# Kernel optimization log

Measured on AMD Instinct MI355X. Metric: run time of the kernel, lower is better.

The kernel has to match this reference:

```python
import jax, jax.numpy as jnp
import numpy as np

B, L, N, D, C, WS, NH = 32, 64, 1024, 512, 8192, 3, 16
HD = D // NH          # head_dim = 32
HID = 2 * D           # MLP expansion = 2


def _ln(x, g, b, eps=1e-5):
    m = jnp.mean(x, -1, keepdims=True)
    v = jnp.mean((x - m) ** 2, -1, keepdims=True)
    return (x - m) * jax.lax.rsqrt(v + eps) * g + b


def setup_inputs() -> dict:
    key = jax.random.key(0)
    ks = jax.random.split(key, 16)
    r = lambda i, shape, s=0.02: jax.random.normal(ks[i], shape, jnp.float32) * s
    return dict(
        visual_features=jax.random.normal(ks[0], (B, N, D), jnp.float32),
        targets=jax.random.randint(ks[1], (B, L), 0, C),
        pad_id=1,
        char_embed=r(2, (C, D), 1.0),
        ln1_g=jnp.ones(D), ln1_b=jnp.zeros(D),
        in_proj_w=r(3, (3 * D, D)), in_proj_b=jnp.zeros(3 * D),
        out_w=r(4, (D, D)), out_b=jnp.zeros(D),
        fc1_w=r(5, (HID, D)), fc1_b=jnp.zeros(HID),
        fc2_w=r(6, (D, HID)), fc2_b=jnp.zeros(D),
        ln2_g=jnp.ones(D), ln2_b=jnp.zeros(D),
        left_token=r(7, (1, 1, D)), right_token=r(8, (1, 1, D)),
        q_w=r(9, (D, D)), q_b=jnp.zeros(D),
        kv_w=r(10, (2 * D, D)), kv_b=jnp.zeros(2 * D),
        proj_w=r(11, (D, D)), proj_b=jnp.zeros(D),
        lnq_g=jnp.ones(D), lnq_b=jnp.zeros(D),
        lnkv_g=jnp.ones(D), lnkv_b=jnp.zeros(D),
        head_w=r(12, (C, D)), head_b=jnp.zeros(C),
    )


def reference(visual_features, targets, pad_id, char_embed, ln1_g, ln1_b,
              in_proj_w, in_proj_b, out_w, out_b, fc1_w, fc1_b, fc2_w, fc2_b,
              ln2_g, ln2_b, left_token, right_token, q_w, q_b, kv_w, kv_b,
              proj_w, proj_b, lnq_g, lnq_b, lnkv_g, lnkv_b, head_w, head_b):
    # --- build left/right context windows via gather (vectorizes the python loop) ---
    padded = jnp.pad(targets, ((0, 0), (WS, WS)), constant_values=pad_id)
    li = jnp.arange(L)[:, None] + jnp.arange(WS)[None, :]      # (L, WS)
    left_ids = padded[:, li]                                   # (B, L, WS)
    right_ids = padded[:, li + WS + 1]                         # (B, L, WS)

    def encode(ids, tok):
        x = char_embed[ids] + tok                 # (B, L, WS, D)
        x = x.reshape(B * L, WS, D)               # (M, WS, D)
        xn = _ln(x, ln1_g, ln1_b)
        qkv = xn @ in_proj_w.T + in_proj_b
        q, k, v = jnp.split(qkv, 3, -1)
        sh = lambda t: t.reshape(B * L, WS, NH, HD).transpose(0, 2, 1, 3)
        q, k, v = sh(q), sh(k), sh(v)
        a = jax.nn.softmax(jnp.einsum('mhqd,mhkd->mhqk', q, k) * HD ** -0.5, -1)
        o = jnp.einsum('mhqk,mhkd->mhqd', a, v).transpose(0, 2, 1, 3).reshape(B * L, WS, D)
        x = x + o @ out_w.T + out_b
        h = jax.nn.gelu(_ln(x, ln2_g, ln2_b) @ fc1_w.T + fc1_b, approximate=False)
        x = x + h @ fc2_w.T + fc2_b
        return x.mean(1).reshape(B, L, D)

    def cross(qs):
        q = _ln(qs, lnq_g, lnq_b) @ q_w.T + q_b
        kv = _ln(visual_features, lnkv_g, lnkv_b) @ kv_w.T + kv_b
        k, v = jnp.split(kv, 2, -1)
        q = q.reshape(B, L, NH, HD).transpose(0, 2, 1, 3)
        k = k.reshape(B, N, NH, HD).transpose(0, 2, 1, 3)
        v = v.reshape(B, N, NH, HD).transpose(0, 2, 1, 3)
        a = jax.nn.softmax(jnp.einsum('bhld,bhnd->bhln', q, k) * HD ** -0.5, -1)
        o = jnp.einsum('bhln,bhnd->bhld', a, v).transpose(0, 2, 1, 3).reshape(B, L, D)
        return o @ proj_w.T + proj_b

    left_enc = encode(left_ids, left_token)
    right_enc = encode(right_ids, right_token)
    left_feat = left_enc + cross(left_enc)
    right_feat = right_enc + cross(right_enc)
    sgm_left = left_feat @ head_w.T + head_b      # (B, L, C)
    sgm_right = right_feat @ head_w.T + head_b    # (B, L, C)
    return sgm_left, sgm_right, targets
```

## Files before the change

### kernel.cpp

```cpp
#include <hip/hip_runtime.h>
#include <hip/hip_bf16.h>
#include <cstdint>
#include <cstddef>


typedef __attribute__((ext_vector_type(8))) short s16x8;
typedef __attribute__((ext_vector_type(8))) unsigned short u16x8;
typedef __attribute__((ext_vector_type(4))) unsigned short u16x4;
typedef __attribute__((ext_vector_type(4))) float f32x4;

__device__ __forceinline__ float b2f(unsigned short u) {
  union { unsigned int i; float f; } c; c.i = ((unsigned int)u) << 16; return c.f;
}
__device__ __forceinline__ unsigned short f2b(float f) {
  union { float f; unsigned int i; } c; c.f = f;
  unsigned int x = c.i;
  return (unsigned short)((x + 0x7FFFu + ((x >> 16) & 1u)) >> 16);
}

#define GLOAD16(gp, lp)                                                        \
  __builtin_amdgcn_global_load_lds(                                           \
      (const __attribute__((address_space(1))) void*)(gp),                    \
      (__attribute__((address_space(3))) void*)(lp), 16, 0, 0)

__global__ void cvt_f32_bf16(const float* __restrict__ s, unsigned short* __restrict__ d, int n4) {
  int i = blockIdx.x * 256 + threadIdx.x;
  if (i >= n4) return;
  float4 v = ((const float4*)s)[i];
  u16x4 o; o[0] = f2b(v.x); o[1] = f2b(v.y); o[2] = f2b(v.z); o[3] = f2b(v.w);
  *(u16x4*)(d + (size_t)i * 4) = o;
}

__global__ void embed_k(const int* __restrict__ targets, const int* __restrict__ pad_p,
                        const float* __restrict__ ce, const float* __restrict__ ltok,
                        const float* __restrict__ rtok, unsigned short* __restrict__ x) {
  int idx = blockIdx.x * 256 + threadIdx.x;
  if (idx >= 12288 * 128) return;
  int row = idx >> 7, d4 = idx & 127;
  int side = row >= 6144;
  int rem = row - side * 6144;
  int pos = rem / 3, w = rem - pos * 3;
  int b = pos >> 6, l = pos & 63;
  int id;
  if (!side) { int ti = l + w - 3; id = (ti >= 0) ? targets[(b << 6) + ti] : *pad_p; }
  else       { int ti = l + w + 1; id = (ti < 64) ? targets[(b << 6) + ti] : *pad_p; }
  float4 cv = ((const float4*)ce)[(size_t)id * 128 + d4];
  float4 tv = ((const float4*)(side ? rtok : ltok))[d4];
  u16x4 o; o[0] = f2b(cv.x + tv.x); o[1] = f2b(cv.y + tv.y);
  o[2] = f2b(cv.z + tv.z); o[3] = f2b(cv.w + tv.w);
  *(u16x4*)(x + (size_t)idx * 4) = o;
}

template<int INBF>
__global__ __launch_bounds__(256) void ln_rows(const void* __restrict__ in,
    const float* __restrict__ g, const float* __restrict__ b,
    unsigned short* __restrict__ out, int M) {
  int row = blockIdx.x * 4 + (threadIdx.x >> 6);
  int lane = threadIdx.x & 63;
  float vv[8];
  if (INBF) {
    u16x8 v8 = *(const u16x8*)((const unsigned short*)in + (size_t)row * 512 + lane * 8);
#pragma unroll
    for (int j = 0; j < 8; ++j) vv[j] = b2f(v8[j]);
  } else {
    const float* rp = (const float*)in + (size_t)row * 512;
    float4 v0 = ((const float4*)rp)[lane * 2];
    float4 v1 = ((const float4*)rp)[lane * 2 + 1];
    vv[0] = v0.x; vv[1] = v0.y; vv[2] = v0.z; vv[3] = v0.w;
    vv[4] = v1.x; vv[5] = v1.y; vv[6] = v1.z; vv[7] = v1.w;
  }
  float s = 0.f, ss = 0.f;
#pragma unroll
  for (int j = 0; j < 8; ++j) { s += vv[j]; ss += vv[j] * vv[j]; }
#pragma unroll
  for (int o = 1; o < 64; o <<= 1) { s += __shfl_xor(s, o); ss += __shfl_xor(ss, o); }
  float mean = s * (1.0f / 512.0f);
  float var = ss * (1.0f / 512.0f) - mean * mean;
  float inv = rsqrtf(var + 1e-5f);
  int c = lane * 8;
  u16x8 o8;
#pragma unroll
  for (int j = 0; j < 8; ++j) o8[j] = f2b((vv[j] - mean) * inv * g[c + j] + b[c + j]);
  *(u16x8*)(out + (size_t)row * 512 + c) = o8;
}

template<int RES, int GELU, int OUTBF, int KVT>
__global__ __launch_bounds__(256) void gemm128(
    const unsigned short* __restrict__ A, const unsigned short* __restrict__ Bt,
    const float* __restrict__ bias, const void* __restrict__ res,
    void* __restrict__ outp, int M, int N, int K) {
  __shared__ unsigned short sA[2][8192];
  __shared__ unsigned short sB[2][8192];
  const int tid = threadIdx.x;
  const int nbx = gridDim.x, nby = gridDim.y;
  int id = blockIdx.y * nbx + blockIdx.x;
  {
    const int nwg = nbx * nby;
    if ((nwg & 7) == 0) id = (id & 7) * (nwg >> 3) + (id >> 3);
  }
  int bm, bn;
  if (nbx >= nby) { bm = (id % nby) * 128; bn = (id / nby) * 128; }
  else            { bm = (id / nbx) * 128; bn = (id % nbx) * 128; }
  const int wave = tid >> 6, lane = tid & 63;
  const int wr = (wave >> 1) * 64, wc = (wave & 1) * 64;
  const int lrow = lane & 15, g = lane >> 4;
  f32x4 acc[4][4] = {};
  const int xoff = (((((lrow & 1) << 2) | g) ^ ((lrow >> 1) & 7)) << 3);
  const int baseA = ((wr >> 1) + (lrow >> 1)) * 64 + xoff;
  const int baseB = ((wc >> 1) + (lrow >> 1)) * 64 + xoff;
  const int slot8 = (tid & 7) ^ ((tid >> 3) & 7);
  const int srow = ((tid >> 3) << 1) + (slot8 >> 2);
  const int scol = (slot8 & 3) << 3;
  const unsigned short* gA = A + (size_t)(bm + srow) * K + scol;
  const unsigned short* gB = Bt + (size_t)(bn + srow) * K + scol;
  const int NT = K >> 6;

#define STAGE128(buf, kt)                                                      \
  { _Pragma("unroll")                                                          \
    for (int h = 0; h < 2; ++h) {                                              \
      _Pragma("unroll")                                                        \
      for (int i = 0; i < 2; ++i) {                                            \
        GLOAD16(gA + (size_t)(i * 64) * K + (kt) * 64 + h * 32,                \
                &sA[buf][h * 4096 + i * 2048 + wave * 512]);                   \
        GLOAD16(gB + (size_t)(i * 64) * K + (kt) * 64 + h * 32,                \
                &sB[buf][h * 4096 + i * 2048 + wave * 512]);                   \
      }                                                                        \
    } }

  STAGE128(0, 0);
  __syncthreads();
  int cur = 0;
  for (int kt = 0; kt < NT; ++kt) {
    s16x8 a0[4], b0[4];
#pragma unroll
    for (int m = 0; m < 4; ++m) a0[m] = *(const s16x8*)&sA[cur][baseA + m * 512];
#pragma unroll
    for (int n = 0; n < 4; ++n) b0[n] = *(const s16x8*)&sB[cur][baseB + n * 512];
    if (kt + 1 < NT) STAGE128(cur ^ 1, kt + 1);
    __builtin_amdgcn_s_setprio(1);
#pragma unroll
    for (int m = 0; m < 4; ++m)
#pragma unroll
      for (int n = 0; n < 4; ++n)
        acc[m][n] = __builtin_amdgcn_mfma_f32_16x16x32_bf16(b0[n], a0[m], acc[m][n], 0, 0, 0);
    __builtin_amdgcn_s_setprio(0);
    s16x8 a1[4], b1[4];
#pragma unroll
    for (int m = 0; m < 4; ++m) a1[m] = *(const s16x8*)&sA[cur][4096 + baseA + m * 512];
#pragma unroll
    for (int n = 0; n < 4; ++n) b1[n] = *(const s16x8*)&sB[cur][4096 + baseB + n * 512];
    __builtin_amdgcn_s_setprio(1);
#pragma unroll
    for (int m = 0; m < 4; ++m)
#pragma unroll
      for (int n = 0; n < 4; ++n)
        acc[m][n] = __builtin_amdgcn_mfma_f32_16x16x32_bf16(b1[n], a1[m], acc[m][n], 0, 0, 0);
    __builtin_amdgcn_s_setprio(0);
    __syncthreads();
    cur ^= 1;
  }
#undef STAGE128

  const int orow_ = bm + wr + lrow;
  const int ocol_ = bn + wc + g * 4;
#pragma unroll
  for (int m = 0; m < 4; ++m) {
    const int row = orow_ + m * 16;
#pragma unroll
    for (int n = 0; n < 4; ++n) {
      const int col = ocol_ + n * 16;
      f32x4 v = acc[m][n];
      f32x4 b4 = *(const f32x4*)(bias + col);
      v += b4;
      if (GELU) {
#pragma unroll
        for (int r = 0; r < 4; ++r)
          v[r] = 0.5f * v[r] * (1.0f + erff(v[r] * 0.70710678118654752f));
      }
      if (RES == 1) v += *(const f32x4*)((const float*)res + (size_t)row * N + col);
      if (RES == 2) {
        u16x4 r4 = *(const u16x4*)((const unsigned short*)res + (size_t)row * N + col);
#pragma unroll
        for (int r = 0; r < 4; ++r) v[r] += b2f(r4[r]);
      }
      if (KVT) {
        int bb = row >> 10, nn = row & 1023;
        unsigned short* Kp = (unsigned short*)outp;
        unsigned short* VpT = Kp + 16777216u;
        if (col < 512) {
          int hh = col >> 5, dd = col & 31;
          u16x4 o4;
#pragma unroll
          for (int r = 0; r < 4; ++r) o4[r] = f2b(v[r]);
          *(u16x4*)(Kp + (((size_t)(bb * 16 + hh)) * 1024 + nn) * 32 + dd) = o4;
        } else {
          int cc = col - 512, hh = cc >> 5, dd = cc & 31;
#pragma unroll
          for (int r = 0; r < 4; ++r)
            VpT[(((size_t)(bb * 16 + hh)) * 32 + dd + r) * 1024 + nn] = f2b(v[r]);
        }
      } else if (OUTBF) {
        u16x4 o4;
#pragma unroll
        for (int r = 0; r < 4; ++r) o4[r] = f2b(v[r]);
        *(u16x4*)((unsigned short*)outp + (size_t)row * N + col) = o4;
      } else {
        *(f32x4*)((float*)outp + (size_t)row * N + col) = v;
      }
    }
  }
}

__global__ __launch_bounds__(256) void winattn(const unsigned short* __restrict__ qkv,
                                               unsigned short* __restrict__ o) {
  int g = blockIdx.x * 256 + threadIdx.x;
  if (g >= 4096 * 48) return;
  int i = g % 3;
  int t = g / 3;
  int h = t & 15;
  int sp = t >> 4;
  const unsigned short* base = qkv + (size_t)sp * 4608 + h * 32;
  float qv[32];
  {
    const u16x8* qp = (const u16x8*)(base + (size_t)i * 1536);
#pragma unroll
    for (int c = 0; c < 4; ++c) {
      u16x8 v = qp[c];
#pragma unroll
      for (int j = 0; j < 8; ++j) qv[c * 8 + j] = b2f(v[j]);
    }
  }
  float s[3];
#pragma unroll
  for (int j3 = 0; j3 < 3; ++j3) {
    const u16x8* kp = (const u16x8*)(base + (size_t)j3 * 1536 + 512);
    float acc = 0.f;
#pragma unroll
    for (int c = 0; c < 4; ++c) {
      u16x8 v = kp[c];
#pragma unroll
      for (int j = 0; j < 8; ++j) acc += qv[c * 8 + j] * b2f(v[j]);
    }
    s[j3] = acc * 0.17677669529663687f;
  }
  float mx = fmaxf(s[0], fmaxf(s[1], s[2]));
  float e0 = __expf(s[0] - mx), e1 = __expf(s[1] - mx), e2 = __expf(s[2] - mx);
  float inv = 1.0f / (e0 + e1 + e2);
  float a0 = e0 * inv, a1 = e1 * inv, a2 = e2 * inv;
  unsigned short* op = o + (size_t)(sp * 3 + i) * 512 + h * 32;
  const u16x8* v0p = (const u16x8*)(base + 1024);
  const u16x8* v1p = (const u16x8*)(base + 1536 + 1024);
  const u16x8* v2p = (const u16x8*)(base + 3072 + 1024);
#pragma unroll
  for (int c = 0; c < 4; ++c) {
    u16x8 x0 = v0p[c], x1 = v1p[c], x2 = v2p[c];
    u16x8 ov;
#pragma unroll
    for (int j = 0; j < 8; ++j)
      ov[j] = f2b(a0 * b2f(x0[j]) + a1 * b2f(x1[j]) + a2 * b2f(x2[j]));
    *(u16x8*)(op + c * 8) = ov;
  }
}

__global__ void mean3(const unsigned short* __restrict__ x, float* __restrict__ enc) {
  int i = blockIdx.x * 256 + threadIdx.x;
  if (i >= 4096 * 128) return;
  int p = i >> 7, d4 = i & 127;
  u16x4 a = *(const u16x4*)(x + ((size_t)(p * 3 + 0) * 512 + d4 * 4));
  u16x4 b = *(const u16x4*)(x + ((size_t)(p * 3 + 1) * 512 + d4 * 4));
  u16x4 c = *(const u16x4*)(x + ((size_t)(p * 3 + 2) * 512 + d4 * 4));
  float4 o;
  o.x = (b2f(a[0]) + b2f(b[0]) + b2f(c[0])) * (1.0f / 3.0f);
  o.y = (b2f(a[1]) + b2f(b[1]) + b2f(c[1])) * (1.0f / 3.0f);
  o.z = (b2f(a[2]) + b2f(b[2]) + b2f(c[2])) * (1.0f / 3.0f);
  o.w = (b2f(a[3]) + b2f(b[3]) + b2f(c[3])) * (1.0f / 3.0f);
  ((float4*)enc)[i] = o;
}

__global__ __launch_bounds__(256) void crossattn_mfma(const unsigned short* __restrict__ q,
    const unsigned short* __restrict__ Kp, const unsigned short* __restrict__ VpT,
    unsigned short* __restrict__ o) {
  __shared__ unsigned short Plds[4][2][16 * 40];
  const int sbh = blockIdx.x;
  const int side = sbh >> 9, b = (sbh >> 4) & 31, h = sbh & 15;
  const int tid = threadIdx.x;
  const int w = tid >> 6, lane = tid & 63;
  const int ql = lane & 15, g = lane >> 4;
  const int qrow = side * 2048 + b * 64 + w * 16 + ql;
  const float SC = 0.17677669529663687f;
  s16x8 qf;
  {
    u16x8 qv8 = *(const u16x8*)(q + (size_t)qrow * 512 + h * 32 + g * 8);
#pragma unroll
    for (int j = 0; j < 8; ++j) qf[j] = (short)f2b(b2f(qv8[j]) * SC);
  }
  const unsigned short* kbase = Kp + ((size_t)(b * 16 + h) * 1024) * 32;
  const unsigned short* vbase = VpT + ((size_t)(b * 16 + h) * 32) * 1024;
  f32x4 oacc0 = {}, oacc1 = {};
  float m_run = -1e30f, l_part = 0.f;
  for (int kv0 = 0; kv0 < 1024; kv0 += 32) {
    const int pp = (kv0 >> 5) & 1;
    s16x8 kf0 = *(const s16x8*)(kbase + (size_t)(kv0 + ql) * 32 + g * 8);
    s16x8 kf1 = *(const s16x8*)(kbase + (size_t)(kv0 + 16 + ql) * 32 + g * 8);
    f32x4 z = {0.f, 0.f, 0.f, 0.f};
    f32x4 s0 = __builtin_amdgcn_mfma_f32_16x16x32_bf16(kf0, qf, z, 0, 0, 0);
    f32x4 s1 = __builtin_amdgcn_mfma_f32_16x16x32_bf16(kf1, qf, z, 0, 0, 0);
    float cm = fmaxf(fmaxf(fmaxf(s0[0], s0[1]), fmaxf(s0[2], s0[3])),
                     fmaxf(fmaxf(s1[0], s1[1]), fmaxf(s1[2], s1[3])));
    cm = fmaxf(cm, __shfl_xor(cm, 16));
    cm = fmaxf(cm, __shfl_xor(cm, 32));
    float m_new = fmaxf(m_run, cm);
    float corr = __expf(m_run - m_new);
    m_run = m_new;
    float p0[4], p1[4], ps = 0.f;
#pragma unroll
    for (int r = 0; r < 4; ++r) {
      p0[r] = __expf(s0[r] - m_new);
      p1[r] = __expf(s1[r] - m_new);
      ps += p0[r] + p1[r];
    }
    l_part = l_part * corr + ps;
    oacc0 *= corr; oacc1 *= corr;
    u16x4 w0, w1;
#pragma unroll
    for (int r = 0; r < 4; ++r) { w0[r] = f2b(p0[r]); w1[r] = f2b(p1[r]); }
    *(u16x4*)&Plds[w][pp][ql * 40 + g * 4] = w0;
    *(u16x4*)&Plds[w][pp][ql * 40 + 16 + g * 4] = w1;
    __syncthreads();
    s16x8 pf = *(const s16x8*)&Plds[w][pp][ql * 40 + g * 8];
    s16x8 vf0 = *(const s16x8*)(vbase + (size_t)ql * 1024 + kv0 + g * 8);
    s16x8 vf1 = *(const s16x8*)(vbase + (size_t)(16 + ql) * 1024 + kv0 + g * 8);
    oacc0 = __builtin_amdgcn_mfma_f32_16x16x32_bf16(vf0, pf, oacc0, 0, 0, 0);
    oacc1 = __builtin_amdgcn_mfma_f32_16x16x32_bf16(vf1, pf, oacc1, 0, 0, 0);
  }
  float lf = l_part;
  lf += __shfl_xor(lf, 16);
  lf += __shfl_xor(lf, 32);
  float inv = 1.0f / lf;
  unsigned short* op = o + (size_t)qrow * 512 + h * 32;
  u16x4 ov0, ov1;
#pragma unroll
  for (int r = 0; r < 4; ++r) {
    ov0[r] = f2b(oacc0[r] * inv);
    ov1[r] = f2b(oacc1[r] * inv);
  }
  *(u16x4*)(op + g * 4) = ov0;
  *(u16x4*)(op + 16 + g * 4) = ov1;
}

__global__ void tail_targets(const int* __restrict__ t, float* __restrict__ out) {
  int i = blockIdx.x * 256 + threadIdx.x;
  if (i < 2048) out[33554432 + i] = (float)t[i];
}

extern "C" void kernel_launch(void* const* d_in, const int* in_sizes, int n_in,
                              void* d_out, int out_size, void* d_ws, size_t ws_size,
                              hipStream_t stream) {
  const float* visual   = (const float*)d_in[0];
  const int*   targets  = (const int*)d_in[1];
  const int*   pad_p    = (const int*)d_in[2];
  const float* char_emb = (const float*)d_in[3];
  const float* ln1_g = (const float*)d_in[4];
  const float* ln1_b = (const float*)d_in[5];
  const float* in_proj_w = (const float*)d_in[6];
  const float* in_proj_b = (const float*)d_in[7];
  const float* out_w = (const float*)d_in[8];
  const float* out_b = (const float*)d_in[9];
  const float* fc1_w = (const float*)d_in[10];
  const float* fc1_b = (const float*)d_in[11];
  const float* fc2_w = (const float*)d_in[12];
  const float* fc2_b = (const float*)d_in[13];
  const float* ln2_g = (const float*)d_in[14];
  const float* ln2_b = (const float*)d_in[15];
  const float* ltok  = (const float*)d_in[16];
  const float* rtok  = (const float*)d_in[17];
  const float* q_w   = (const float*)d_in[18];
  const float* q_b   = (const float*)d_in[19];
  const float* kv_w  = (const float*)d_in[20];
  const float* kv_b  = (const float*)d_in[21];
  const float* proj_w = (const float*)d_in[22];
  const float* proj_b = (const float*)d_in[23];
  const float* lnq_g = (const float*)d_in[24];
  const float* lnq_b = (const float*)d_in[25];
  const float* lnkv_g = (const float*)d_in[26];
  const float* lnkv_b = (const float*)d_in[27];
  const float* head_w = (const float*)d_in[28];
  const float* head_b = (const float*)d_in[29];

  char* ws = (char*)d_ws;
  unsigned short* W    = (unsigned short*)ws;
  unsigned short* XB   = (unsigned short*)(ws + 14680064ull);
  unsigned short* KP   = (unsigned short*)(ws + 14680064ull);
  unsigned short* A1   = (unsigned short*)(ws + 39845888ull);
  unsigned short* B1   = (unsigned short*)(ws + 52428800ull);
  unsigned short* QKV  = (unsigned short*)(ws + 77594624ull);
  float*          ENC  = (float*)(ws + 115343360ull);
  unsigned short* VIS  = (unsigned short*)(ws + 123731968ull);
  unsigned short* Q    = (unsigned short*)(ws + 157286400ull);
  unsigned short* OC   = (unsigned short*)(ws + 165675008ull);
  unsigned short* FEAT = (unsigned short*)(ws + 169869312ull);
  unsigned short* LNQ  = (unsigned short*)(ws + 174063616ull);
  unsigned short* VPT  = KP + 16777216u;

  unsigned short* Wip   = W;
  unsigned short* Wout  = W + 786432;
  unsigned short* Wfc1  = W + 1048576;
  unsigned short* Wfc2  = W + 1572864;
  unsigned short* Wq    = W + 2097152;
  unsigned short* Wkv   = W + 2359296;
  unsigned short* Wproj = W + 2883584;
  unsigned short* Whead = W + 3145728;

  auto cvt = [&](const float* s, unsigned short* d, int n) {
    cvt_f32_bf16<<<dim3((n / 4 + 255) / 256), dim3(256), 0, stream>>>(s, d, n / 4);
  };
  cvt(in_proj_w, Wip, 786432);
  cvt(out_w, Wout, 262144);
  cvt(fc1_w, Wfc1, 524288);
  cvt(fc2_w, Wfc2, 524288);
  cvt(q_w, Wq, 262144);
  cvt(kv_w, Wkv, 524288);
  cvt(proj_w, Wproj, 262144);
  cvt(head_w, Whead, 4194304);

  embed_k<<<dim3(6144), dim3(256), 0, stream>>>(targets, pad_p, char_emb, ltok, rtok, XB);
  ln_rows<1><<<dim3(3072), dim3(256), 0, stream>>>(XB, ln1_g, ln1_b, A1, 12288);
  gemm128<0,0,1,0><<<dim3(12, 96), dim3(256), 0, stream>>>(A1, Wip, in_proj_b, nullptr, QKV, 12288, 1536, 512);
  winattn<<<dim3(768), dim3(256), 0, stream>>>(QKV, B1);
  gemm128<2,0,1,0><<<dim3(4, 96), dim3(256), 0, stream>>>(B1, Wout, out_b, XB, XB, 12288, 512, 512);
  ln_rows<1><<<dim3(3072), dim3(256), 0, stream>>>(XB, ln2_g, ln2_b, A1, 12288);
  gemm128<0,1,1,0><<<dim3(8, 96), dim3(256), 0, stream>>>(A1, Wfc1, fc1_b, nullptr, B1, 12288, 1024, 512);
  gemm128<2,0,1,0><<<dim3(4, 96), dim3(256), 0, stream>>>(B1, Wfc2, fc2_b, XB, XB, 12288, 512, 1024);
  mean3<<<dim3(2048), dim3(256), 0, stream>>>(XB, ENC);

  ln_rows<0><<<dim3(8192), dim3(256), 0, stream>>>(visual, lnkv_g, lnkv_b, VIS, 32768);
  gemm128<0,0,1,1><<<dim3(8, 256), dim3(256), 0, stream>>>(VIS, Wkv, kv_b, nullptr, KP, 32768, 1024, 512);
  ln_rows<0><<<dim3(1024), dim3(256), 0, stream>>>(ENC, lnq_g, lnq_b, LNQ, 4096);
  gemm128<0,0,1,0><<<dim3(4, 32), dim3(256), 0, stream>>>(LNQ, Wq, q_b, nullptr, Q, 4096, 512, 512);
  crossattn_mfma<<<dim3(1024), dim3(256), 0, stream>>>(Q, KP, VPT, OC);
  gemm128<1,0,1,0><<<dim3(4, 32), dim3(256), 0, stream>>>(OC, Wproj, proj_b, ENC, FEAT, 4096, 512, 512);

  gemm128<0,0,0,0><<<dim3(64, 32), dim3(256), 0, stream>>>(FEAT, Whead, head_b, nullptr, (float*)d_out, 4096, 8192, 512);
  tail_targets<<<dim3(8), dim3(256), 0, stream>>>(targets, (float*)d_out);
}
```

Before: 416.9 us.

## Merge weight conversions, fuse both sides into one cross-attn block, simplify GEMM tile mapping

Replaces eight separate f32-to-bf16 weight conversion launches with one kernel that picks the source buffer by offset, cutting launch overhead. Cross-attention now runs 512-thread blocks covering both left and right sides for a (batch, head), so each block walks the same K/V slice for both sides and can reuse it through cache. The GEMM block-to-tile mapping drops the branch on grid shape and always maps row-major over gridDim.x, which changes tile traversal order and L2 locality for tall grids.

```diff
diff --git a/kernel.cpp b/kernel.cpp
--- a/kernel.cpp
+++ b/kernel.cpp
@@ -23,12 +23,26 @@
       (const __attribute__((address_space(1))) void*)(gp),                    \
       (__attribute__((address_space(3))) void*)(lp), 16, 0, 0)
 
-__global__ void cvt_f32_bf16(const float* __restrict__ s, unsigned short* __restrict__ d, int n4) {
-  int i = blockIdx.x * 256 + threadIdx.x;
-  if (i >= n4) return;
-  float4 v = ((const float4*)s)[i];
+__global__ void cvt_all(const float* __restrict__ s0, const float* __restrict__ s1,
+                        const float* __restrict__ s2, const float* __restrict__ s3,
+                        const float* __restrict__ s4, const float* __restrict__ s5,
+                        const float* __restrict__ s6, const float* __restrict__ s7,
+                        unsigned short* __restrict__ d) {
+  int c = blockIdx.x * 256 + threadIdx.x;
+  if (c >= 1835008) return;
+  int e = c * 4;
+  const float* sp; int off;
+  if      (e <  786432) { sp = s0; off = 0; }
+  else if (e < 1048576) { sp = s1; off =  786432; }
+  else if (e < 1572864) { sp = s2; off = 1048576; }
+  else if (e < 2097152) { sp = s3; off = 1572864; }
+  else if (e < 2359296) { sp = s4; off = 2097152; }
+  else if (e < 2883584) { sp = s5; off = 2359296; }
+  else if (e < 3145728) { sp = s6; off = 2883584; }
+  else                  { sp = s7; off = 3145728; }
+  float4 v = *(const float4*)(sp + (e - off));
   u16x4 o; o[0] = f2b(v.x); o[1] = f2b(v.y); o[2] = f2b(v.z); o[3] = f2b(v.w);
-  *(u16x4*)(d + (size_t)i * 4) = o;
+  *(u16x4*)(d + e) = o;
 }
 
 __global__ void embed_k(const int* __restrict__ targets, const int* __restrict__ pad_p,
@@ -92,15 +106,13 @@
   __shared__ unsigned short sA[2][8192];
   __shared__ unsigned short sB[2][8192];
   const int tid = threadIdx.x;
-  const int nbx = gridDim.x, nby = gridDim.y;
+  const int nbx = gridDim.x;
   int id = blockIdx.y * nbx + blockIdx.x;
   {
-    const int nwg = nbx * nby;
+    const int nwg = nbx * gridDim.y;
     if ((nwg & 7) == 0) id = (id & 7) * (nwg >> 3) + (id >> 3);
   }
-  int bm, bn;
-  if (nbx >= nby) { bm = (id % nby) * 128; bn = (id / nby) * 128; }
-  else            { bm = (id / nbx) * 128; bn = (id % nbx) * 128; }
+  const int bm = (id / nbx) * 128, bn = (id % nbx) * 128;
   const int wave = tid >> 6, lane = tid & 63;
   const int wr = (wave >> 1) * 64, wc = (wave & 1) * 64;
   const int lrow = lane & 15, g = lane >> 4;
@@ -277,16 +289,17 @@
   ((float4*)enc)[i] = o;
 }
 
-__global__ __launch_bounds__(256) void crossattn_mfma(const unsigned short* __restrict__ q,
+__global__ __launch_bounds__(512) void crossattn_mfma(const unsigned short* __restrict__ q,
     const unsigned short* __restrict__ Kp, const unsigned short* __restrict__ VpT,
     unsigned short* __restrict__ o) {
-  __shared__ unsigned short Plds[4][2][16 * 40];
-  const int sbh = blockIdx.x;
-  const int side = sbh >> 9, b = (sbh >> 4) & 31, h = sbh & 15;
+  __shared__ unsigned short Plds[8][2][16 * 40];
+  const int bh = blockIdx.x;
+  const int b = bh >> 4, h = bh & 15;
   const int tid = threadIdx.x;
   const int w = tid >> 6, lane = tid & 63;
+  const int side = w >> 2, wsub = w & 3;
   const int ql = lane & 15, g = lane >> 4;
-  const int qrow = side * 2048 + b * 64 + w * 16 + ql;
+  const int qrow = side * 2048 + b * 64 + wsub * 16 + ql;
   const float SC = 0.17677669529663687f;
   s16x8 qf;
   {
@@ -403,25 +416,16 @@
   unsigned short* VPT  = KP + 16777216u;
 
   unsigned short* Wip   = W;
-  unsigned short* Wout  = W + 786432;
   unsigned short* Wfc1  = W + 1048576;
   unsigned short* Wfc2  = W + 1572864;
   unsigned short* Wq    = W + 2097152;
   unsigned short* Wkv   = W + 2359296;
   unsigned short* Wproj = W + 2883584;
   unsigned short* Whead = W + 3145728;
-
-  auto cvt = [&](const float* s, unsigned short* d, int n) {
-    cvt_f32_bf16<<<dim3((n / 4 + 255) / 256), dim3(256), 0, stream>>>(s, d, n / 4);
-  };
-  cvt(in_proj_w, Wip, 786432);
-  cvt(out_w, Wout, 262144);
-  cvt(fc1_w, Wfc1, 524288);
-  cvt(fc2_w, Wfc2, 524288);
-  cvt(q_w, Wq, 262144);
-  cvt(kv_w, Wkv, 524288);
-  cvt(proj_w, Wproj, 262144);
-  cvt(head_w, Whead, 4194304);
+  unsigned short* Wout  = W + 786432;
+
+  cvt_all<<<dim3(7168), dim3(256), 0, stream>>>(in_proj_w, out_w, fc1_w, fc2_w,
+                                                q_w, kv_w, proj_w, head_w, W);
 
   embed_k<<<dim3(6144), dim3(256), 0, stream>>>(targets, pad_p, char_emb, ltok, rtok, XB);
   ln_rows<1><<<dim3(3072), dim3(256), 0, stream>>>(XB, ln1_g, ln1_b, A1, 12288);
@@ -437,7 +441,7 @@
   gemm128<0,0,1,1><<<dim3(8, 256), dim3(256), 0, stream>>>(VIS, Wkv, kv_b, nullptr, KP, 32768, 1024, 512);
   ln_rows<0><<<dim3(1024), dim3(256), 0, stream>>>(ENC, lnq_g, lnq_b, LNQ, 4096);
   gemm128<0,0,1,0><<<dim3(4, 32), dim3(256), 0, stream>>>(LNQ, Wq, q_b, nullptr, Q, 4096, 512, 512);
-  crossattn_mfma<<<dim3(1024), dim3(256), 0, stream>>>(Q, KP, VPT, OC);
+  crossattn_mfma<<<dim3(512), dim3(512), 0, stream>>>(Q, KP, VPT, OC);
   gemm128<1,0,1,0><<<dim3(4, 32), dim3(256), 0, stream>>>(OC, Wproj, proj_b, ENC, FEAT, 4096, 512, 512);
 
   gemm128<0,0,0,0><<<dim3(64, 32), dim3(256), 0, stream>>>(FEAT, Whead, head_b, nullptr, (float*)d_out, 4096, 8192, 512);
```

Result: faster. 390.3 us (-6.4%).
